# Kernel optimization log

Hardware: AMD Instinct MI355X
Metric: run time of the kernel (lower is better)

## Reference

```python
import jax, jax.numpy as jnp
import numpy as np
from jax import lax

DN = ('NCHW', 'OIHW', 'NCHW')

def conv3x3(x, w):
    return lax.conv_general_dilated(x, w, (1, 1), 'SAME', dimension_numbers=DN)

def conv1x1(x, w, b):
    # w: [O, C], x: [B, C, H, W]
    return jnp.einsum('oc,bchw->bohw', w, x) + b[None, :, None, None]

def bn_relu(x, p):
    # p: [2, C] -> (scale, shift), eval-mode folded BatchNorm + ReLU
    return jax.nn.relu(x * p[0][None, :, None, None] + p[1][None, :, None, None])

def pam(y, Wb, bb, Wc, bc, Wd, bd, alpha):
    B, C, H, W = y.shape
    n = H * W
    b_ = conv1x1(y, Wb, bb).reshape(B, -1, n)   # [B, C/8, N]
    c_ = conv1x1(y, Wc, bc).reshape(B, -1, n)   # [B, C/8, N]
    d_ = conv1x1(y, Wd, bd).reshape(B, C, n)    # [B, C, N]
    energy = jnp.einsum('bkn,bkm->bnm', b_, c_)  # [B, N, N]
    attn = jax.nn.softmax(energy, axis=-1)
    feat = jnp.einsum('bcm,bnm->bcn', d_, attn).reshape(B, C, H, W)
    return alpha[0] * feat + y

def cam(y, beta):
    B, C, H, W = y.shape
    xf = y.reshape(B, C, H * W)
    energy = jnp.einsum('bcn,bdn->bcd', xf, xf)  # [B, C, C]
    energy = jnp.max(energy, axis=-1, keepdims=True) - energy
    attn = jax.nn.softmax(energy, axis=-1)
    feat = jnp.einsum('bcd,bdn->bcn', attn, xf).reshape(B, C, H, W)
    return beta[0] * feat + y

def reference(x, Wp1, bnp1, Wc1, bnc1, Wb, bb, Wc, bc, Wd, bd, alpha, beta,
              Wp2, bnp2, Wc2, bnc2, Wout, bout, Wp3, bp3, Wc3, bc3):
    feat_p = bn_relu(conv3x3(x, Wp1), bnp1)
    feat_p = pam(feat_p, Wb, bb, Wc, bc, Wd, bd, alpha)
    feat_p = bn_relu(conv3x3(feat_p, Wp2), bnp2)

    feat_c = bn_relu(conv3x3(x, Wc1), bnc1)
    feat_c = cam(feat_c, beta)
    feat_c = bn_relu(conv3x3(feat_c, Wc2), bnc2)

    fusion = feat_p + feat_c
    out_main = jax.nn.sigmoid(conv1x1(fusion, Wout, bout))
    out_p = jax.nn.sigmoid(conv1x1(feat_p, Wp3, bp3))
    out_c = jax.nn.sigmoid(conv1x1(feat_c, Wc3, bc3))
    return (out_main, out_p, out_c)

def setup_inputs() -> dict:
    key = jax.random.key(0)
    ks = jax.random.split(key, 24)
    Cin, Ci, Ck, NC = 512, 128, 16, 19
    B, H, W = 8, 64, 64
    s = lambda k, shape, scale=0.05: jax.random.normal(k, shape, jnp.float32) * scale
    return {
        'x': jax.random.normal(ks[0], (B, Cin, H, W), jnp.float32),
        'Wp1': s(ks[1], (Ci, Cin, 3, 3)), 'bnp1': jnp.stack([jnp.ones(Ci), jnp.zeros(Ci)]),
        'Wc1': s(ks[2], (Ci, Cin, 3, 3)), 'bnc1': jnp.stack([jnp.ones(Ci), jnp.zeros(Ci)]),
        'Wb': s(ks[3], (Ck, Ci)), 'bb': s(ks[4], (Ck,)),
        'Wc': s(ks[5], (Ck, Ci)), 'bc': s(ks[6], (Ck,)),
        'Wd': s(ks[7], (Ci, Ci)), 'bd': s(ks[8], (Ci,)),
        'alpha': jax.random.normal(ks[9], (1,), jnp.float32) * 0.5,
        'beta': jax.random.normal(ks[10], (1,), jnp.float32) * 0.5,
        'Wp2': s(ks[11], (Ci, Ci, 3, 3)), 'bnp2': jnp.stack([jnp.ones(Ci), jnp.zeros(Ci)]),
        'Wc2': s(ks[12], (Ci, Ci, 3, 3)), 'bnc2': jnp.stack([jnp.ones(Ci), jnp.zeros(Ci)]),
        'Wout': s(ks[13], (NC, Ci)), 'bout': s(ks[14], (NC,)),
        'Wp3': s(ks[15], (NC, Ci)), 'bp3': s(ks[16], (NC,)),
        'Wc3': s(ks[17], (NC, Ci)), 'bc3': s(ks[18], (NC,)),
    }
```

## Files before the change

### kernel.cpp

```cpp
#include <hip/hip_runtime.h>
#include <math.h>


typedef __attribute__((ext_vector_type(8)))  short short8;
typedef __attribute__((ext_vector_type(16))) float f32x16;

__device__ inline unsigned short f2bf(float f) {
    union { float f; unsigned u; } v; v.f = f;
    unsigned r = v.u + 0x7fffu + ((v.u >> 16) & 1u);
    return (unsigned short)(r >> 16);
}
__device__ inline float bf2f(unsigned short h) {
    union { unsigned u; float f; } v; v.u = ((unsigned)h) << 16;
    return v.f;
}

__global__ __launch_bounds__(256) void wpack_kernel(
    const float* __restrict__ W, unsigned short* __restrict__ wp, int Cin, int total)
{
    int idx = blockIdx.x * 256 + threadIdx.x;
    if (idx >= total) return;
    int chunk = idx / 18432;
    int rem   = idx - chunk * 18432;
    int tap   = rem >> 11;
    int rem2  = rem & 2047;
    int co    = rem2 >> 4;
    int ci    = rem2 & 15;
    int cin   = (chunk << 4) + ci;
    wp[idx] = f2bf(W[((size_t)co * Cin + cin) * 9 + tap]);
}

__global__ __launch_bounds__(256) void wpack_split_kernel(
    const float* __restrict__ W, unsigned short* __restrict__ wph,
    unsigned short* __restrict__ wpl, int Cin, int total)
{
    int idx = blockIdx.x * 256 + threadIdx.x;
    if (idx >= total) return;
    int chunk = idx / 18432;
    int rem   = idx - chunk * 18432;
    int tap   = rem >> 11;
    int rem2  = rem & 2047;
    int co    = rem2 >> 4;
    int ci    = rem2 & 15;
    int cin   = (chunk << 4) + ci;
    float w = W[((size_t)co * Cin + cin) * 9 + tap];
    unsigned short hi = f2bf(w);
    wph[idx] = hi;
    wpl[idx] = f2bf(w - bf2f(hi));
}

__global__ __launch_bounds__(256) void x_split_kernel(
    const float* __restrict__ x, unsigned short* __restrict__ xh,
    unsigned short* __restrict__ xl)
{
    const int ch = blockIdx.x;
    const int b  = blockIdx.y;
    const int t  = threadIdx.x;
    for (int seg = 0; seg < 16; ++seg) {
        const int n = (seg << 8) + t;
        unsigned short uh[16], ul[16];
#pragma unroll
        for (int c = 0; c < 16; ++c) {
            float f = x[(((size_t)b * 512 + (ch << 4) + c) << 12) + n];
            unsigned short hi = f2bf(f);
            uh[c] = hi;
            ul[c] = f2bf(f - bf2f(hi));
        }
        size_t dst = ((((size_t)b * 32 + ch) << 12) + n) << 4;
        *(uint4*)(xh + dst)     = ((uint4*)uh)[0];
        *(uint4*)(xh + dst + 8) = ((uint4*)uh)[1];
        *(uint4*)(xl + dst)     = ((uint4*)ul)[0];
        *(uint4*)(xl + dst + 8) = ((uint4*)ul)[1];
    }
}

__global__ __launch_bounds__(256) void conv3x3_mfma(
    const unsigned short* __restrict__ xb, int Cin,
    const unsigned short* __restrict__ wpack, const float* __restrict__ bn,
    float* __restrict__ out_f32)
{
    const int t   = threadIdx.x;
    const int w   = t >> 6;
    const int wy  = w >> 1;
    const int wx  = w & 1;
    const int ln  = t & 63;
    const int l31 = ln & 31;
    const int g   = ln >> 5;
    const int y0  = blockIdx.x << 1;
    const int co0 = blockIdx.y << 6;
    const int b   = blockIdx.z;
    const int nc16 = Cin >> 4;

    __shared__ __align__(16) unsigned short Xl[4 * 66 * 16];
    __shared__ __align__(16) unsigned short Wl[9 * 64 * 16];

    if (t < 8) {
        int r = t >> 1, xc = (t & 1) * 65;
        uint4 z = {0, 0, 0, 0};
        *(uint4*)&Xl[(r * 66 + xc) * 16 + 0] = z;
        *(uint4*)&Xl[(r * 66 + xc) * 16 + 8] = z;
    }

    const f32x16 zero = {0,0,0,0,0,0,0,0,0,0,0,0,0,0,0,0};
    f32x16 acc0 = zero, acc1 = zero;

    for (int ch = 0; ch < nc16; ++ch) {
#pragma unroll
        for (int it = 0; it < 2; ++it) {
            int idx = t + (it << 8);
            int r = idx >> 7, u = idx & 127;
            int gy = y0 - 1 + r;
            uint4 val = {0, 0, 0, 0};
            if ((unsigned)gy < 64u)
                val = *(const uint4*)(xb + ((((size_t)(b * nc16 + ch)) << 12) + (gy << 6)) * 16 + (u << 3));
            *(uint4*)&Xl[(r * 66 + 1) * 16 + (u << 3)] = val;
        }
        {
            const uint4* wsrc = (const uint4*)wpack;
            const int base = ch * 2304 + (co0 << 1);
            for (int idx = t; idx < 1152; idx += 256)
                ((uint4*)Wl)[idx] = wsrc[base + ((idx >> 7) << 8) + (idx & 127)];
        }
        __syncthreads();

#pragma unroll 3
        for (int tap = 0; tap < 9; ++tap) {
            const int dy = tap / 3, dx = tap - dy * 3;
            short8 a = *(const short8*)&Wl[((tap << 6) + (wy << 5) + l31) * 16 + (g << 3)];
            const int row = wx + dy;
            short8 b0 = *(const short8*)&Xl[(row * 66 + l31 + dx) * 16 + (g << 3)];
            short8 b1 = *(const short8*)&Xl[(row * 66 + l31 + 32 + dx) * 16 + (g << 3)];
            acc0 = __builtin_amdgcn_mfma_f32_32x32x16_bf16(a, b0, acc0, 0, 0, 0);
            acc1 = __builtin_amdgcn_mfma_f32_32x32x16_bf16(a, b1, acc1, 0, 0, 0);
        }
        __syncthreads();
    }

    const int y = y0 + wx;
#pragma unroll
    for (int j = 0; j < 2; j++) {
        const f32x16 a = j ? acc1 : acc0;
#pragma unroll
        for (int r = 0; r < 16; r++) {
            int co = co0 + (wy << 5) + (r & 3) + ((r >> 2) << 3) + (g << 2);
            int x  = (j << 5) + l31;
            float v = fmaf(a[r], bn[co], bn[128 + co]);
            v = v > 0.f ? v : 0.f;
            out_f32[(((size_t)b * 128 + co) << 12) + (y << 6) + x] = v;
        }
    }
}

__global__ __launch_bounds__(256) void conv3x3_mfma_hilo(
    const unsigned short* __restrict__ xbh, const unsigned short* __restrict__ xbl,
    int Cin, const unsigned short* __restrict__ wph, const unsigned short* __restrict__ wpl,
    const float* __restrict__ bn, float* __restrict__ out_f32,
    unsigned short* __restrict__ outh, unsigned short* __restrict__ outl)
{
    const int t   = threadIdx.x;
    const int w   = t >> 6;
    const int wy  = w >> 1;
    const int wx  = w & 1;
    const int ln  = t & 63;
    const int l31 = ln & 31;
    const int g   = ln >> 5;
    const int y0  = blockIdx.x << 1;
    const int co0 = blockIdx.y << 6;
    const int b   = blockIdx.z;
    const int nc16 = Cin >> 4;

    __shared__ __align__(16) unsigned short Xh[4 * 66 * 16];
    __shared__ __align__(16) unsigned short Xo[4 * 66 * 16];
    __shared__ __align__(16) unsigned short Wh[9 * 64 * 16];
    __shared__ __align__(16) unsigned short Wo[9 * 64 * 16];

    if (t < 8) {
        int r = t >> 1, xc = (t & 1) * 65;
        uint4 z = {0, 0, 0, 0};
        *(uint4*)&Xh[(r * 66 + xc) * 16 + 0] = z;
        *(uint4*)&Xh[(r * 66 + xc) * 16 + 8] = z;
        *(uint4*)&Xo[(r * 66 + xc) * 16 + 0] = z;
        *(uint4*)&Xo[(r * 66 + xc) * 16 + 8] = z;
    }

    const f32x16 zero = {0,0,0,0,0,0,0,0,0,0,0,0,0,0,0,0};
    f32x16 acc0 = zero, acc1 = zero;

    for (int ch = 0; ch < nc16; ++ch) {
#pragma unroll
        for (int it = 0; it < 2; ++it) {
            int idx = t + (it << 8);
            int r = idx >> 7, u = idx & 127;
            int gy = y0 - 1 + r;
            uint4 vh = {0, 0, 0, 0}, vl = {0, 0, 0, 0};
            if ((unsigned)gy < 64u) {
                size_t o = ((((size_t)(b * nc16 + ch)) << 12) + (gy << 6)) * 16 + (u << 3);
                vh = *(const uint4*)(xbh + o);
                vl = *(const uint4*)(xbl + o);
            }
            *(uint4*)&Xh[(r * 66 + 1) * 16 + (u << 3)] = vh;
            *(uint4*)&Xo[(r * 66 + 1) * 16 + (u << 3)] = vl;
        }
        {
            const uint4* sh = (const uint4*)wph;
            const uint4* sl = (const uint4*)wpl;
            const int base = ch * 2304 + (co0 << 1);
            for (int idx = t; idx < 1152; idx += 256) {
                int o = base + ((idx >> 7) << 8) + (idx & 127);
                ((uint4*)Wh)[idx] = sh[o];
                ((uint4*)Wo)[idx] = sl[o];
            }
        }
        __syncthreads();

#pragma unroll 1
        for (int tap = 0; tap < 9; ++tap) {
            const int dy = tap / 3, dx = tap - dy * 3;
            const int wi = ((tap << 6) + (wy << 5) + l31) * 16 + (g << 3);
            const int row = wx + dy;
            const int xi0 = (row * 66 + l31 + dx) * 16 + (g << 3);
            const int xi1 = (row * 66 + l31 + 32 + dx) * 16 + (g << 3);
            short8 ah = *(const short8*)&Wh[wi];
            short8 al = *(const short8*)&Wo[wi];
            short8 b0h = *(const short8*)&Xh[xi0];
            short8 b1h = *(const short8*)&Xh[xi1];
            short8 b0l = *(const short8*)&Xo[xi0];
            short8 b1l = *(const short8*)&Xo[xi1];
            acc0 = __builtin_amdgcn_mfma_f32_32x32x16_bf16(ah, b0h, acc0, 0, 0, 0);
            acc1 = __builtin_amdgcn_mfma_f32_32x32x16_bf16(ah, b1h, acc1, 0, 0, 0);
            acc0 = __builtin_amdgcn_mfma_f32_32x32x16_bf16(ah, b0l, acc0, 0, 0, 0);
            acc1 = __builtin_amdgcn_mfma_f32_32x32x16_bf16(ah, b1l, acc1, 0, 0, 0);
            acc0 = __builtin_amdgcn_mfma_f32_32x32x16_bf16(al, b0h, acc0, 0, 0, 0);
            acc1 = __builtin_amdgcn_mfma_f32_32x32x16_bf16(al, b1h, acc1, 0, 0, 0);
        }
        __syncthreads();
    }

    const int y = y0 + wx;
#pragma unroll
    for (int j = 0; j < 2; j++) {
        const f32x16 a = j ? acc1 : acc0;
#pragma unroll
        for (int r = 0; r < 16; r++) {
            int co = co0 + (wy << 5) + (r & 3) + ((r >> 2) << 3) + (g << 2);
            int x  = (j << 5) + l31;
            float v = fmaf(a[r], bn[co], bn[128 + co]);
            v = v > 0.f ? v : 0.f;
            size_t o = (((size_t)b * 128 + co) << 12) + (y << 6) + x;
            if (out_f32) out_f32[o] = v;
            if (outh) {
                unsigned short hi = f2bf(v);
                outh[o] = hi;
                outl[o] = f2bf(v - bf2f(hi));
            }
        }
    }
}

__global__ __launch_bounds__(256) void cam_energy_mfma(
    const unsigned short* __restrict__ bh, const unsigned short* __restrict__ bl,
    float* __restrict__ egy_part)
{
    const int t   = threadIdx.x;
    const int w   = t >> 6;
    const int ln  = t & 63;
    const int l31 = ln & 31;
    const int g   = ln >> 5;
    const int i0  = (blockIdx.x >> 2) << 5;
    const int j0  = (blockIdx.x & 3) << 5;
    const int nseg = blockIdx.y;
    const int b   = blockIdx.z;

    __shared__ float red[4][64][17];

    const f32x16 zero = {0,0,0,0,0,0,0,0,0,0,0,0,0,0,0,0};
    f32x16 acc = zero;
    const int nb = (nseg << 9) + (w << 7) + (g << 3);
    const size_t ri = ((size_t)b * 128 + i0 + l31) << 12;
    const size_t rj = ((size_t)b * 128 + j0 + l31) << 12;

#pragma unroll
    for (int c = 0; c < 8; c++) {
        const int n0 = nb + (c << 4);
        short8 ah  = *(const short8*)(bh + ri + n0);
        short8 al  = *(const short8*)(bl + ri + n0);
        short8 bhf = *(const short8*)(bh + rj + n0);
        short8 blf = *(const short8*)(bl + rj + n0);
        acc = __builtin_amdgcn_mfma_f32_32x32x16_bf16(ah, bhf, acc, 0, 0, 0);
        acc = __builtin_amdgcn_mfma_f32_32x32x16_bf16(ah, blf, acc, 0, 0, 0);
        acc = __builtin_amdgcn_mfma_f32_32x32x16_bf16(al, bhf, acc, 0, 0, 0);
    }
#pragma unroll
    for (int r = 0; r < 16; r++) red[w][ln][r] = acc[r];
    __syncthreads();

    const int lane = t & 63;
    const int rq   = t >> 6;
    float* base = egy_part + (((size_t)(nseg * 8 + b)) << 14);
#pragma unroll
    for (int e = 0; e < 4; e++) {
        const int reg = (rq << 2) + e;
        float v = red[0][lane][reg] + red[1][lane][reg]
                + red[2][lane][reg] + red[3][lane][reg];
        const int i = i0 + (reg & 3) + ((reg >> 2) << 3) + ((lane >> 5) << 2);
        base[i * 128 + j0 + (lane & 31)] = v;
    }
}

__global__ __launch_bounds__(256) void cam_softmax_fused(
    const float* __restrict__ egy_part, float* __restrict__ egy)
{
    const int b   = blockIdx.x;
    const int rg  = blockIdx.y;
    const int t   = threadIdx.x;
    const int row = (rg << 4) + (t >> 4);
    const int jg  = t & 15;

    float e[8];
#pragma unroll
    for (int jj = 0; jj < 8; jj++) e[jj] = 0.f;
    for (int seg = 0; seg < 8; seg++) {
        const float* p = egy_part + (((size_t)(seg * 8 + b)) << 14) + row * 128 + (jg << 3);
#pragma unroll
        for (int jj = 0; jj < 8; jj++) e[jj] += p[jj];
    }
    float mn = e[0];
#pragma unroll
    for (int jj = 1; jj < 8; jj++) mn = fminf(mn, e[jj]);
#pragma unroll
    for (int k = 1; k < 16; k <<= 1) mn = fminf(mn, __shfl_xor(mn, k));
    float s = 0.f;
#pragma unroll
    for (int jj = 0; jj < 8; jj++) { float p = __expf(mn - e[jj]); e[jj] = p; s += p; }
#pragma unroll
    for (int k = 1; k < 16; k <<= 1) s += __shfl_xor(s, k);
    const float inv = 1.f / s;
    float* orow = egy + ((size_t)b << 14) + row * 128 + (jg << 3);
#pragma unroll
    for (int jj = 0; jj < 8; jj++) orow[jj] = e[jj] * inv;
}

__global__ __launch_bounds__(256) void pam_qk_1x1(
    const float* __restrict__ A, const float* __restrict__ Wb, const float* __restrict__ bb,
    const float* __restrict__ Wc, const float* __restrict__ bc,
    unsigned short* __restrict__ qt, unsigned short* __restrict__ kt)
{
    __shared__ float wl[2 * 16 * 128];
    __shared__ float bl[32];
    const int t = threadIdx.x;
    const int n = (blockIdx.x << 8) + t;
    const int b = blockIdx.y;
    for (int idx = t; idx < 2048; idx += 256) { wl[idx] = Wb[idx]; wl[2048 + idx] = Wc[idx]; }
    if (t < 16) { bl[t] = bb[t]; bl[16 + t] = bc[t]; }
    __syncthreads();
    float ab[16], ac[16];
#pragma unroll
    for (int k = 0; k < 16; k++) { ab[k] = 0.f; ac[k] = 0.f; }
    for (int chn = 0; chn < 128; ++chn) {
        float a = A[(((size_t)b * 128 + chn) << 12) + n];
#pragma unroll
        for (int k = 0; k < 16; k++) {
            ab[k] = fmaf(wl[k * 128 + chn], a, ab[k]);
            ac[k] = fmaf(wl[2048 + k * 128 + chn], a, ac[k]);
        }
    }
    unsigned short uq[16], uk[16];
#pragma unroll
    for (int k = 0; k < 16; k++) {
        uq[k] = f2bf(ab[k] + bl[k]);
        uk[k] = f2bf(ac[k] + bl[16 + k]);
    }
    size_t row = (size_t)b * 4096 + n;
    ((uint4*)qt)[row * 2 + 0] = ((uint4*)uq)[0];
    ((uint4*)qt)[row * 2 + 1] = ((uint4*)uq)[1];
    ((uint4*)kt)[row * 2 + 0] = ((uint4*)uk)[0];
    ((uint4*)kt)[row * 2 + 1] = ((uint4*)uk)[1];
}

__global__ __launch_bounds__(256) void pam_v_1x1(
    const float* __restrict__ A, const float* __restrict__ Wd, const float* __restrict__ bd,
    unsigned short* __restrict__ vb)
{
    __shared__ float wl[32 * 128];
    __shared__ float bl[32];
    const int t   = threadIdx.x;
    const int n   = (blockIdx.x << 8) + t;
    const int co0 = blockIdx.y << 5;
    const int b   = blockIdx.z;
    for (int idx = t; idx < 4096; idx += 256) {
        int c2 = idx >> 7, chv = idx & 127;
        wl[idx] = Wd[(co0 + c2) * 128 + chv];
    }
    if (t < 32) bl[t] = bd[co0 + t];
    __syncthreads();
    float acc[32];
#pragma unroll
    for (int k = 0; k < 32; k++) acc[k] = 0.f;
    for (int chn = 0; chn < 128; ++chn) {
        float a = A[(((size_t)b * 128 + chn) << 12) + n];
#pragma unroll
        for (int k = 0; k < 32; k++) acc[k] = fmaf(wl[k * 128 + chn], a, acc[k]);
    }
#pragma unroll
    for (int k = 0; k < 32; k++)
        vb[(((size_t)b * 128 + co0 + k) << 12) + n] = f2bf(acc[k] + bl[k]);
}

__global__ __launch_bounds__(256) void pam_rowmax(
    const unsigned short* __restrict__ qt, const unsigned short* __restrict__ kt,
    float* __restrict__ rowmax)
{
    const int t  = threadIdx.x;
    const int w  = t >> 6;
    const int L  = t & 63;
    const int ln = L & 31;
    const int g  = L >> 5;
    const int b  = blockIdx.y;
    const int n0 = blockIdx.x << 5;
    __shared__ float red[4][32];

    const f32x16 zero = {0,0,0,0,0,0,0,0,0,0,0,0,0,0,0,0};
    short8 qfrag = *(const short8*)(qt + (((size_t)b * 4096 + n0 + ln) << 4) + (g << 3));

    float mx = -INFINITY;
    for (int mq = (w << 5); mq < 4096; mq += 128) {
        short8 kfrag = *(const short8*)(kt + (((size_t)b * 4096 + mq + ln) << 4) + (g << 3));
        f32x16 s = __builtin_amdgcn_mfma_f32_32x32x16_bf16(kfrag, qfrag, zero, 0, 0, 0);
#pragma unroll
        for (int r = 0; r < 16; r++) mx = fmaxf(mx, s[r]);
    }
    mx = fmaxf(mx, __shfl_xor(mx, 32));
    if (L < 32) red[w][L] = mx;
    __syncthreads();
    if (t < 32) {
        float m = fmaxf(fmaxf(red[0][t], red[1][t]), fmaxf(red[2][t], red[3][t]));
        rowmax[((size_t)b << 12) + n0 + t] = m;
    }
}

__global__ __launch_bounds__(256) void pam_attn_mfma(
    const unsigned short* __restrict__ qt, const unsigned short* __restrict__ kt,
    const unsigned short* __restrict__ vb, const float* __restrict__ rowmax,
    const float* __restrict__ alpha, const float* __restrict__ Y,
    unsigned short* __restrict__ outb)
{
    const int t  = threadIdx.x;
    const int w  = t >> 6;
    const int L  = t & 63;
    const int ln = L & 31;
    const int g  = L >> 5;
    const int b  = blockIdx.y;
    const int n0 = blockIdx.x << 5;
    const int c0 = w << 5;

    __shared__ unsigned short Pf[16 * 256];
    __shared__ float red[4][32];

    const f32x16 zero = {0,0,0,0,0,0,0,0,0,0,0,0,0,0,0,0};
    short8 qfrag = *(const short8*)(qt + (((size_t)b * 4096 + n0 + ln) << 4) + (g << 3));
    const float rm = rowmax[((size_t)b << 12) + n0 + ln];
    const float al = alpha[0];

    f32x16 acc = zero;
    float rs = 0.f;

    for (int m0 = 0; m0 < 4096; m0 += 128) {
        const int mq = m0 + (w << 5);
        short8 kfrag = *(const short8*)(kt + (((size_t)b * 4096 + mq + ln) << 4) + (g << 3));
        f32x16 s = __builtin_amdgcn_mfma_f32_32x32x16_bf16(kfrag, qfrag, zero, 0, 0, 0);

        float p[16];
#pragma unroll
        for (int r = 0; r < 16; r++) { p[r] = __expf(s[r] - rm); rs += p[r]; }
        float xx[16];
#pragma unroll
        for (int r = 0; r < 16; r++) xx[r] = __shfl_xor(p[r], 32);

        unsigned short f0[8], f1[8];
#pragma unroll
        for (int i = 0; i < 4; i++) {
            f0[i]     = f2bf(g ? xx[4 + i]  : p[i]);
            f0[4 + i] = f2bf(g ? p[4 + i]   : xx[i]);
            f1[i]     = f2bf(g ? xx[12 + i] : p[8 + i]);
            f1[4 + i] = f2bf(g ? p[12 + i]  : xx[8 + i]);
        }
        *(short8*)(&Pf[((w << 2) + g) * 256 + (ln << 3)])     = *(short8*)f0;
        *(short8*)(&Pf[((w << 2) + 2 + g) * 256 + (ln << 3)]) = *(short8*)f1;
        __syncthreads();

#pragma unroll
        for (int kk = 0; kk < 8; kk++) {
            short8 pfrag = *(const short8*)(&Pf[((kk << 1) + g) * 256 + (ln << 3)]);
            short8 vfrag = *(const short8*)(vb + (((size_t)b * 128 + c0 + ln) << 12)
                                               + m0 + (kk << 4) + (g << 3));
            acc = __builtin_amdgcn_mfma_f32_32x32x16_bf16(vfrag, pfrag, acc, 0, 0, 0);
        }
        __syncthreads();
    }

    rs += __shfl_xor(rs, 32);
    if (L < 32) red[w][L] = rs;
    __syncthreads();
    const float inv = 1.f / (red[0][ln] + red[1][ln] + red[2][ln] + red[3][ln]);
    const int n = n0 + ln;
#pragma unroll
    for (int r = 0; r < 16; r++) {
        int c = c0 + (r & 3) + ((r >> 2) << 3) + (g << 2);
        size_t yi = (((size_t)b * 128 + c) << 12) + n;
        size_t oo = ((((size_t)b * 8 + (c >> 4)) << 12) + n) * 16 + (c & 15);
        outb[oo] = f2bf(fmaf(al, acc[r] * inv, Y[yi]));
    }
}

__global__ __launch_bounds__(256) void cam_feat(
    const float* __restrict__ attn, const unsigned short* __restrict__ bh,
    const unsigned short* __restrict__ blo, const float* __restrict__ beta,
    unsigned short* __restrict__ camh, unsigned short* __restrict__ caml)
{
    const int t  = threadIdx.x;
    const int n  = (blockIdx.x << 8) + t;
    const int c0 = blockIdx.y << 5;
    const int b  = blockIdx.z;
    __shared__ float al[32 * 128];
    for (int idx = t; idx < 4096; idx += 256)
        al[idx] = attn[((size_t)b << 14) + (c0 + (idx >> 7)) * 128 + (idx & 127)];
    __syncthreads();
    float acc[32];
#pragma unroll
    for (int k = 0; k < 32; k++) acc[k] = 0.f;
    for (int d = 0; d < 128; ++d) {
        size_t idx = (((size_t)b * 128 + d) << 12) + n;
        float v = bf2f(bh[idx]) + bf2f(blo[idx]);
#pragma unroll
        for (int k = 0; k < 32; k++) acc[k] = fmaf(al[k * 128 + d], v, acc[k]);
    }
    float be = beta[0];
    unsigned short oh[32], ol[32];
#pragma unroll
    for (int k = 0; k < 32; k++) {
        size_t idx = (((size_t)b * 128 + c0 + k) << 12) + n;
        float bfv = bf2f(bh[idx]) + bf2f(blo[idx]);
        float v = fmaf(be, acc[k], bfv);
        unsigned short hi = f2bf(v);
        oh[k] = hi;
        ol[k] = f2bf(v - bf2f(hi));
    }
    const int g0 = c0 >> 4;
    size_t d0 = ((((size_t)b * 8 + g0) << 12) + n) << 4;
    size_t d1 = ((((size_t)b * 8 + g0 + 1) << 12) + n) << 4;
    *(uint4*)(camh + d0)     = ((uint4*)oh)[0];
    *(uint4*)(camh + d0 + 8) = ((uint4*)oh)[1];
    *(uint4*)(camh + d1)     = ((uint4*)oh)[2];
    *(uint4*)(camh + d1 + 8) = ((uint4*)oh)[3];
    *(uint4*)(caml + d0)     = ((uint4*)ol)[0];
    *(uint4*)(caml + d0 + 8) = ((uint4*)ol)[1];
    *(uint4*)(caml + d1)     = ((uint4*)ol)[2];
    *(uint4*)(caml + d1 + 8) = ((uint4*)ol)[3];
}

__global__ __launch_bounds__(256) void heads(
    const float* __restrict__ FP, const float* __restrict__ FC,
    const float* __restrict__ Wout, const float* __restrict__ bout,
    const float* __restrict__ Wp3, const float* __restrict__ bp3,
    const float* __restrict__ Wc3, const float* __restrict__ bc3,
    float* __restrict__ out)
{
    const int t = threadIdx.x;
    const int n = (blockIdx.x << 8) + t;
    const int b = blockIdx.y;
    __shared__ float wl[3 * 19 * 128];
    __shared__ float bl[3 * 19];
    for (int idx = t; idx < 2432; idx += 256) {
        wl[idx]        = Wout[idx];
        wl[2432 + idx] = Wp3[idx];
        wl[4864 + idx] = Wc3[idx];
    }
    if (t < 19) { bl[t] = bout[t]; bl[19 + t] = bp3[t]; bl[38 + t] = bc3[t]; }
    __syncthreads();
    float am[19], ap[19], ac[19];
#pragma unroll
    for (int o = 0; o < 19; o++) { am[o] = 0.f; ap[o] = 0.f; ac[o] = 0.f; }
    for (int chn = 0; chn < 128; ++chn) {
        float pv = FP[(((size_t)b * 128 + chn) << 12) + n];
        float cv = FC[(((size_t)b * 128 + chn) << 12) + n];
        float fv = pv + cv;
#pragma unroll
        for (int o = 0; o < 19; o++) {
            am[o] = fmaf(wl[o * 128 + chn], fv, am[o]);
            ap[o] = fmaf(wl[2432 + o * 128 + chn], pv, ap[o]);
            ac[o] = fmaf(wl[4864 + o * 128 + chn], cv, ac[o]);
        }
    }
    const size_t OS = (size_t)8 * 19 * 4096;
#pragma unroll
    for (int o = 0; o < 19; o++) {
        size_t base = (((size_t)b * 19 + o) << 12) + n;
        out[base]          = 1.f / (1.f + __expf(-(am[o] + bl[o])));
        out[OS + base]     = 1.f / (1.f + __expf(-(ap[o] + bl[19 + o])));
        out[2 * OS + base] = 1.f / (1.f + __expf(-(ac[o] + bl[38 + o])));
    }
}

extern "C" void kernel_launch(void* const* d_in, const int* in_sizes, int n_in,
                              void* d_out, int out_size, void* d_ws, size_t ws_size,
                              hipStream_t stream)
{
    const float* x     = (const float*)d_in[0];
    const float* Wp1   = (const float*)d_in[1];
    const float* bnp1  = (const float*)d_in[2];
    const float* Wc1   = (const float*)d_in[3];
    const float* bnc1  = (const float*)d_in[4];
    const float* Wb    = (const float*)d_in[5];
    const float* bb    = (const float*)d_in[6];
    const float* Wc    = (const float*)d_in[7];
    const float* bcv   = (const float*)d_in[8];
    const float* Wd    = (const float*)d_in[9];
    const float* bd    = (const float*)d_in[10];
    const float* alpha = (const float*)d_in[11];
    const float* beta  = (const float*)d_in[12];
    const float* Wp2   = (const float*)d_in[13];
    const float* bnp2  = (const float*)d_in[14];
    const float* Wc2   = (const float*)d_in[15];
    const float* bnc2  = (const float*)d_in[16];
    const float* Wout  = (const float*)d_in[17];
    const float* bo    = (const float*)d_in[18];
    const float* Wp3   = (const float*)d_in[19];
    const float* bp3   = (const float*)d_in[20];
    const float* Wc3   = (const float*)d_in[21];
    const float* bc3   = (const float*)d_in[22];
    float* out = (float*)d_out;

    char* ws = (char*)d_ws;
    const size_t MB = 1u << 20;
    const size_t W1SZ = (size_t)32 * 18432 * 2;
    const size_t W2SZ = (size_t)8 * 18432 * 2;
    float*          bufA     = (float*)(ws);
    unsigned short* bh       = (unsigned short*)(ws + 16 * MB);
    unsigned short* blo      = (unsigned short*)(ws + 24 * MB);
    unsigned short* xh       = (unsigned short*)(ws + 32 * MB);
    unsigned short* xl       = (unsigned short*)(ws + 64 * MB);
    float*          egy_part = (float*)(ws + 32 * MB);
    unsigned short* qt       = (unsigned short*)(ws + 36 * MB);
    unsigned short* kt       = (unsigned short*)(ws + 37 * MB);
    float*          rowmax   = (float*)(ws + 38 * MB);
    float*          egy      = (float*)(ws + 38 * MB + (1u << 18));
    unsigned short* vb       = (unsigned short*)(ws + 40 * MB);
    float*          bufD     = (float*)(ws + 48 * MB);
    unsigned short* pam_bfB  = (unsigned short*)(ws + 64 * MB);
    unsigned short* camh     = (unsigned short*)(ws + 72 * MB);
    unsigned short* caml     = (unsigned short*)(ws + 80 * MB);
    unsigned short* wp1      = (unsigned short*)(ws + 96 * MB);
    unsigned short* wc1h     = (unsigned short*)(ws + 96 * MB + W1SZ);
    unsigned short* wc1l     = (unsigned short*)(ws + 96 * MB + 2 * W1SZ);
    unsigned short* wp2      = (unsigned short*)(ws + 96 * MB + 3 * W1SZ);
    unsigned short* wc2h     = (unsigned short*)(ws + 96 * MB + 3 * W1SZ + W2SZ);
    unsigned short* wc2l     = (unsigned short*)(ws + 96 * MB + 3 * W1SZ + 2 * W2SZ);

    dim3 blk(256);
    const int n1 = 32 * 18432;
    const int n2 = 8 * 18432;
    wpack_kernel<<<dim3((n1 + 255) / 256), blk, 0, stream>>>(Wp1, wp1, 512, n1);
    wpack_kernel<<<dim3((n2 + 255) / 256), blk, 0, stream>>>(Wp2, wp2, 128, n2);
    wpack_split_kernel<<<dim3((n1 + 255) / 256), blk, 0, stream>>>(Wc1, wc1h, wc1l, 512, n1);
    wpack_split_kernel<<<dim3((n2 + 255) / 256), blk, 0, stream>>>(Wc2, wc2h, wc2l, 128, n2);

    x_split_kernel<<<dim3(32, 8), blk, 0, stream>>>(x, xh, xl);

    conv3x3_mfma<<<dim3(32, 2, 8), blk, 0, stream>>>(xh, 512, wp1, bnp1, bufA);
    conv3x3_mfma_hilo<<<dim3(32, 2, 8), blk, 0, stream>>>(xh, xl, 512, wc1h, wc1l, bnc1,
                                                          (float*)0, bh, blo);
    cam_energy_mfma<<<dim3(16, 8, 8), blk, 0, stream>>>(bh, blo, egy_part);
    cam_softmax_fused<<<dim3(8, 8), blk, 0, stream>>>(egy_part, egy);
    pam_qk_1x1<<<dim3(16, 8), blk, 0, stream>>>(bufA, Wb, bb, Wc, bcv, qt, kt);
    pam_v_1x1<<<dim3(16, 4, 8), blk, 0, stream>>>(bufA, Wd, bd, vb);
    pam_rowmax<<<dim3(128, 8), blk, 0, stream>>>(qt, kt, rowmax);
    pam_attn_mfma<<<dim3(128, 8), blk, 0, stream>>>(qt, kt, vb, rowmax, alpha, bufA, pam_bfB);
    conv3x3_mfma<<<dim3(32, 2, 8), blk, 0, stream>>>(pam_bfB, 128, wp2, bnp2, bufD);
    cam_feat<<<dim3(16, 4, 8), blk, 0, stream>>>(egy, bh, blo, beta, camh, caml);
    conv3x3_mfma_hilo<<<dim3(32, 2, 8), blk, 0, stream>>>(camh, caml, 128, wc2h, wc2l, bnc2,
                                                          bufA, (unsigned short*)0, (unsigned short*)0);
    heads<<<dim3(16, 8), blk, 0, stream>>>(bufD, bufA, Wout, bo, Wp3, bp3, Wc3, bc3, out);
}
```

Before: 893.4 us.

## Split PAM attention over key halves and blocked V layout with combine kernel

The PAM attention kernel now splits the key dimension into two halves across a new grid axis, doubling block count. Each half writes unnormalized partial outputs and row sums to fp32 buffers. A new combine kernel then sums them, normalizes, applies alpha plus the residual, and writes the blocked bf16 output. V is also stored in a 16-wide blocked layout so the MFMA fragment loads are contiguous. The cost is extra fp32 partial traffic (about 32MB written and read) and one more launch.

```diff
diff --git a/kernel.cpp b/kernel.cpp
--- a/kernel.cpp
+++ b/kernel.cpp
@@ -379,7 +379,7 @@
 
 __global__ __launch_bounds__(256) void pam_v_1x1(
     const float* __restrict__ A, const float* __restrict__ Wd, const float* __restrict__ bd,
-    unsigned short* __restrict__ vb)
+    unsigned short* __restrict__ vbB)
 {
     __shared__ float wl[32 * 128];
     __shared__ float bl[32];
@@ -401,9 +401,10 @@
 #pragma unroll
         for (int k = 0; k < 32; k++) acc[k] = fmaf(wl[k * 128 + chn], a, acc[k]);
     }
+    const size_t mbase = (((size_t)b * 256 + (n >> 4)) * 128 + co0) * 16 + (n & 15);
 #pragma unroll
     for (int k = 0; k < 32; k++)
-        vb[(((size_t)b * 128 + co0 + k) << 12) + n] = f2bf(acc[k] + bl[k]);
+        vbB[mbase + (size_t)k * 16] = f2bf(acc[k] + bl[k]);
 }
 
 __global__ __launch_bounds__(256) void pam_rowmax(
@@ -440,16 +441,16 @@
 
 __global__ __launch_bounds__(256) void pam_attn_mfma(
     const unsigned short* __restrict__ qt, const unsigned short* __restrict__ kt,
-    const unsigned short* __restrict__ vb, const float* __restrict__ rowmax,
-    const float* __restrict__ alpha, const float* __restrict__ Y,
-    unsigned short* __restrict__ outb)
+    const unsigned short* __restrict__ vbB, const float* __restrict__ rowmax,
+    float* __restrict__ part, float* __restrict__ lsum)
 {
     const int t  = threadIdx.x;
     const int w  = t >> 6;
     const int L  = t & 63;
     const int ln = L & 31;
     const int g  = L >> 5;
-    const int b  = blockIdx.y;
+    const int mh = blockIdx.y;
+    const int b  = blockIdx.z;
     const int n0 = blockIdx.x << 5;
     const int c0 = w << 5;
 
@@ -459,12 +460,12 @@
     const f32x16 zero = {0,0,0,0,0,0,0,0,0,0,0,0,0,0,0,0};
     short8 qfrag = *(const short8*)(qt + (((size_t)b * 4096 + n0 + ln) << 4) + (g << 3));
     const float rm = rowmax[((size_t)b << 12) + n0 + ln];
-    const float al = alpha[0];
 
     f32x16 acc = zero;
     float rs = 0.f;
 
-    for (int m0 = 0; m0 < 4096; m0 += 128) {
+    const int mbeg = mh << 11;
+    for (int m0 = mbeg; m0 < mbeg + 2048; m0 += 128) {
         const int mq = m0 + (w << 5);
         short8 kfrag = *(const short8*)(kt + (((size_t)b * 4096 + mq + ln) << 4) + (g << 3));
         f32x16 s = __builtin_amdgcn_mfma_f32_32x32x16_bf16(kfrag, qfrag, zero, 0, 0, 0);
@@ -488,11 +489,12 @@
         *(short8*)(&Pf[((w << 2) + 2 + g) * 256 + (ln << 3)]) = *(short8*)f1;
         __syncthreads();
 
+        const int mc0 = m0 >> 4;
 #pragma unroll
         for (int kk = 0; kk < 8; kk++) {
             short8 pfrag = *(const short8*)(&Pf[((kk << 1) + g) * 256 + (ln << 3)]);
-            short8 vfrag = *(const short8*)(vb + (((size_t)b * 128 + c0 + ln) << 12)
-                                               + m0 + (kk << 4) + (g << 3));
+            short8 vfrag = *(const short8*)(vbB + (((size_t)b * 256 + mc0 + kk) * 128
+                                                    + c0 + ln) * 16 + (g << 3));
             acc = __builtin_amdgcn_mfma_f32_32x32x16_bf16(vfrag, pfrag, acc, 0, 0, 0);
         }
         __syncthreads();
@@ -501,14 +503,42 @@
     rs += __shfl_xor(rs, 32);
     if (L < 32) red[w][L] = rs;
     __syncthreads();
-    const float inv = 1.f / (red[0][ln] + red[1][ln] + red[2][ln] + red[3][ln]);
+    if (t < 32)
+        lsum[(((size_t)(mh * 8 + b)) << 12) + n0 + t]
+            = red[0][t] + red[1][t] + red[2][t] + red[3][t];
+
     const int n = n0 + ln;
 #pragma unroll
     for (int r = 0; r < 16; r++) {
         int c = c0 + (r & 3) + ((r >> 2) << 3) + (g << 2);
-        size_t yi = (((size_t)b * 128 + c) << 12) + n;
-        size_t oo = ((((size_t)b * 8 + (c >> 4)) << 12) + n) * 16 + (c & 15);
-        outb[oo] = f2bf(fmaf(al, acc[r] * inv, Y[yi]));
+        part[((((size_t)(mh * 8 + b)) * 128 + c) << 12) + n] = acc[r];
+    }
+}
+
+__global__ __launch_bounds__(256) void pam_combine(
+    const float* __restrict__ part, const float* __restrict__ lsum,
+    const float* __restrict__ alpha, const float* __restrict__ Y,
+    unsigned short* __restrict__ outb)
+{
+    const int t = threadIdx.x;
+    const int n = (blockIdx.x << 8) + t;
+    const int b = blockIdx.y;
+    const size_t h1 = (size_t)8 * 128 * 4096;
+    const float l = lsum[((size_t)b << 12) + n] + lsum[(((size_t)(8 + b)) << 12) + n];
+    const float sc = alpha[0] / l;
+#pragma unroll 1
+    for (int cg = 0; cg < 8; ++cg) {
+        unsigned short o[16];
+#pragma unroll
+        for (int j = 0; j < 16; ++j) {
+            const int c = (cg << 4) + j;
+            const size_t idx = (((size_t)b * 128 + c) << 12) + n;
+            float v = fmaf(sc, part[idx] + part[h1 + idx], Y[idx]);
+            o[j] = f2bf(v);
+        }
+        size_t dst = ((((size_t)b * 8 + cg) << 12) + n) << 4;
+        *(uint4*)(outb + dst)     = ((uint4*)o)[0];
+        *(uint4*)(outb + dst + 8) = ((uint4*)o)[1];
     }
 }
 
@@ -643,12 +673,14 @@
     unsigned short* qt       = (unsigned short*)(ws + 36 * MB);
     unsigned short* kt       = (unsigned short*)(ws + 37 * MB);
     float*          rowmax   = (float*)(ws + 38 * MB);
-    float*          egy      = (float*)(ws + 38 * MB + (1u << 18));
-    unsigned short* vb       = (unsigned short*)(ws + 40 * MB);
-    float*          bufD     = (float*)(ws + 48 * MB);
-    unsigned short* pam_bfB  = (unsigned short*)(ws + 64 * MB);
-    unsigned short* camh     = (unsigned short*)(ws + 72 * MB);
-    unsigned short* caml     = (unsigned short*)(ws + 80 * MB);
+    float*          egy      = (float*)(ws + 38 * MB + (1u << 17));
+    unsigned short* vbB      = (unsigned short*)(ws + 39 * MB);
+    float*          part     = (float*)(ws + 47 * MB);
+    float*          lsum     = (float*)(ws + 79 * MB);
+    unsigned short* pam_bfB  = (unsigned short*)(ws + 80 * MB);
+    float*          bufD     = (float*)(ws + 47 * MB);
+    unsigned short* camh     = (unsigned short*)(ws + 63 * MB);
+    unsigned short* caml     = (unsigned short*)(ws + 71 * MB);
     unsigned short* wp1      = (unsigned short*)(ws + 96 * MB);
     unsigned short* wc1h     = (unsigned short*)(ws + 96 * MB + W1SZ);
     unsigned short* wc1l     = (unsigned short*)(ws + 96 * MB + 2 * W1SZ);
@@ -671,13 +703,18 @@
                                                           (float*)0, bh, blo);
     cam_energy_mfma<<<dim3(16, 8, 8), blk, 0, stream>>>(bh, blo, egy_part);
     cam_softmax_fused<<<dim3(8, 8), blk, 0, stream>>>(egy_part, egy);
+
     pam_qk_1x1<<<dim3(16, 8), blk, 0, stream>>>(bufA, Wb, bb, Wc, bcv, qt, kt);
-    pam_v_1x1<<<dim3(16, 4, 8), blk, 0, stream>>>(bufA, Wd, bd, vb);
+    pam_v_1x1<<<dim3(16, 4, 8), blk, 0, stream>>>(bufA, Wd, bd, vbB);
     pam_rowmax<<<dim3(128, 8), blk, 0, stream>>>(qt, kt, rowmax);
-    pam_attn_mfma<<<dim3(128, 8), blk, 0, stream>>>(qt, kt, vb, rowmax, alpha, bufA, pam_bfB);
+    pam_attn_mfma<<<dim3(128, 2, 8), blk, 0, stream>>>(qt, kt, vbB, rowmax, part, lsum);
+    pam_combine<<<dim3(16, 8), blk, 0, stream>>>(part, lsum, alpha, bufA, pam_bfB);
+
     conv3x3_mfma<<<dim3(32, 2, 8), blk, 0, stream>>>(pam_bfB, 128, wp2, bnp2, bufD);
+
     cam_feat<<<dim3(16, 4, 8), blk, 0, stream>>>(egy, bh, blo, beta, camh, caml);
     conv3x3_mfma_hilo<<<dim3(32, 2, 8), blk, 0, stream>>>(camh, caml, 128, wc2h, wc2l, bnc2,
                                                           bufA, (unsigned short*)0, (unsigned short*)0);
+
     heads<<<dim3(16, 8), blk, 0, stream>>>(bufD, bufA, Wout, bo, Wp3, bp3, Wc3, bc3, out);
 }
```

After: 866.2 us. 1.03x faster.
